# Optimization experiments

Measured on AMD Instinct MI355X. Metric: run time of the kernel, lower is better.

Reference implementation:

```python
import math
import jax, jax.numpy as jnp
import numpy as np

B, S, T = 16, 1024, 2048
C, Fdim = 128, 20          # C*Fdim = 2560 (q in_features)
PH_DIM = 512               # k/v in_features
OUT_DIM = 512              # out_dim
MEL_DIM = 20 * 64          # 1280


def setup_inputs() -> dict:
    key = jax.random.key(0)
    ks = jax.random.split(key, 12)
    ph = jax.random.normal(ks[0], (B, S, PH_DIM), dtype=jnp.float32)
    g = jax.random.normal(ks[1], (B, C, Fdim, T), dtype=jnp.float32)
    lengths = jax.random.randint(ks[2], (B,), 1, S + 1, dtype=jnp.int64)
    def lin(k, fan_in, fan_out):
        bound = 1.0 / math.sqrt(fan_in)
        kw, kb = jax.random.split(k)
        W = jax.random.uniform(kw, (fan_in, fan_out), jnp.float32, -bound, bound)
        b = jax.random.uniform(kb, (fan_out,), jnp.float32, -bound, bound)
        return W, b
    Wk, bk = lin(ks[3], PH_DIM, OUT_DIM)
    Wv, bv = lin(ks[4], PH_DIM, OUT_DIM)
    Wq, bq = lin(ks[5], C * Fdim, OUT_DIM)
    Wmel, bmel = lin(ks[6], OUT_DIM, MEL_DIM)
    return {"ph": ph, "g": g, "lengths": lengths,
            "Wk": Wk, "bk": bk, "Wv": Wv, "bv": bv,
            "Wq": Wq, "bq": bq, "Wmel": Wmel, "bmel": bmel}


def reference(ph, g, lengths, Wk, bk, Wv, bv, Wq, bq, Wmel, bmel):
    b, c, f, t = g.shape
    d = Wk.shape[1]
    k = ph @ Wk + bk                              # [B,S,D]
    q = g.reshape(b, c * f, t).transpose(0, 2, 1) @ Wq + bq  # [B,T,D]
    att = jnp.einsum('btd,bsd->bts', q, k) / math.sqrt(d)    # [B,T,S]
    valid = jnp.arange(k.shape[1])[None, None, :] < lengths[:, None, None]
    att = jnp.where(valid, att, -jnp.inf)
    att = jax.nn.softmax(att, axis=2)
    v = ph @ Wv + bv                              # [B,S,D]
    value = jnp.einsum('bts,bsd->btd', att, v)    # [B,T,D]
    out = value @ Wmel + bmel                     # [B,T,1280]
    out = out.reshape(b, t, f, -1).transpose(0, 3, 2, 1)  # [B,64,F,T]
    return out
```

## Files before the change

### kernel.cpp

```cpp
#include <hip/hip_runtime.h>
#include <stdint.h>


typedef __attribute__((ext_vector_type(4))) float f32x4;
typedef __attribute__((ext_vector_type(8))) short bf16x8;

#define AS1 __attribute__((address_space(1)))
#define AS3 __attribute__((address_space(3)))

__device__ __forceinline__ ushort f2b(float x) {
    union { float f; uint32_t u; } v; v.f = x;
    uint32_t r = (v.u + 0x7FFFu + ((v.u >> 16) & 1u)) >> 16;
    return (ushort)r;
}
__device__ __forceinline__ float b2f(ushort u) {
    union { uint32_t u; float f; } v; v.u = ((uint32_t)u) << 16;
    return v.f;
}

__device__ __forceinline__ void gload16(const void* g, void* l) {
    __builtin_amdgcn_global_load_lds((const AS1 uint32_t*)g,
                                     (AS3 uint32_t*)l, 16, 0, 0);
}

__global__ void sniff_dtype(const uint32_t* __restrict__ ph, int* __restrict__ flag)
{
    if (threadIdx.x == 0 && blockIdx.x == 0) {
        int cnt = 0;
        for (int i = 0; i < 64; ++i) {
            uint32_t e = (ph[i] >> 7) & 0xFFu;
            if (e >= 90u && e <= 140u) ++cnt;
        }
        *flag = (cnt >= 40) ? 1 : 0;
    }
}


__global__ __launch_bounds__(256)
void cvt_bias(const void* __restrict__ src, float* __restrict__ dst, int n,
              const int* __restrict__ flag)
{
    int i = blockIdx.x * 256 + threadIdx.x;
    if (i >= n) return;
    dst[i] = (*flag == 0) ? ((const float*)src)[i]
                          : b2f(((const ushort*)src)[i]);
}

__global__ __launch_bounds__(256)
void cvt_bf16(const void* __restrict__ src, ushort* __restrict__ dst, int n8,
              const int* __restrict__ flag)
{
    int i = blockIdx.x * 256 + threadIdx.x;
    if (i >= n8) return;
    if (*flag == 0) {
        const float4* s = (const float4*)src;
        float4 a = s[2 * i], b = s[2 * i + 1];
        uint4 o;
        o.x = (uint32_t)f2b(a.x) | ((uint32_t)f2b(a.y) << 16);
        o.y = (uint32_t)f2b(a.z) | ((uint32_t)f2b(a.w) << 16);
        o.z = (uint32_t)f2b(b.x) | ((uint32_t)f2b(b.y) << 16);
        o.w = (uint32_t)f2b(b.z) | ((uint32_t)f2b(b.w) << 16);
        ((uint4*)dst)[i] = o;
    } else {
        ((uint4*)dst)[i] = ((const uint4*)src)[i];
    }
}

__global__ __launch_bounds__(256)
void transpose_cvt(const void* __restrict__ src, ushort* __restrict__ dst,
                   int R, int Cc, long sbat, long dbat,
                   const int* __restrict__ flag)
{
    __shared__ ushort tile[32][33];
    const bool isf32 = (*flag == 0);
    const int r0 = blockIdx.y * 32, c0 = blockIdx.x * 32;
    const int tr = threadIdx.x >> 3;
    const int tc4 = (threadIdx.x & 7) * 4;

    const char* sb = (const char*)src + (size_t)blockIdx.z * sbat * (isf32 ? 4 : 2);
    if (isf32) {
        const float4* s = (const float4*)((const float*)sb + (size_t)(r0 + tr) * Cc + c0 + tc4);
        float4 v = *s;
        tile[tr][tc4 + 0] = f2b(v.x); tile[tr][tc4 + 1] = f2b(v.y);
        tile[tr][tc4 + 2] = f2b(v.z); tile[tr][tc4 + 3] = f2b(v.w);
    } else {
        const ushort4* s = (const ushort4*)((const ushort*)sb + (size_t)(r0 + tr) * Cc + c0 + tc4);
        ushort4 v = *s;
        tile[tr][tc4 + 0] = v.x; tile[tr][tc4 + 1] = v.y;
        tile[tr][tc4 + 2] = v.z; tile[tr][tc4 + 3] = v.w;
    }
    __syncthreads();
    ushort4 o;
    o.x = tile[tc4 + 0][tr]; o.y = tile[tc4 + 1][tr];
    o.z = tile[tc4 + 2][tr]; o.w = tile[tc4 + 3][tr];
    *(ushort4*)(dst + (size_t)blockIdx.z * dbat + (size_t)(c0 + tr) * R + r0 + tc4) = o;
}

template<int STORE>
__global__ __launch_bounds__(256)
void mfma_gemm(const ushort* __restrict__ A, const ushort* __restrict__ Bt,
               void* __restrict__ C, const float* __restrict__ bias,
               int M, int N, int K,
               long Abat, long Bbat, long Cbat, long ldc, float scale)
{
    __shared__ ushort As[128 * 32];
    __shared__ ushort Bs[128 * 32];

    const int tid = threadIdx.x;
    const int lane = tid & 63;
    const int wave = tid >> 6;
    const int wr = wave >> 1, wc = wave & 1;
    const int m0 = blockIdx.y * 128, n0 = blockIdx.x * 128;

    const ushort* Ab = A + (size_t)blockIdx.z * Abat;
    const ushort* Bb = Bt + (size_t)blockIdx.z * Bbat;

    const int srow = tid >> 2;
    const int scol = (tid & 3) * 8;
    const ushort* gA = Ab + (size_t)(m0 + srow) * K + scol;
    const ushort* gB = Bb + (size_t)(n0 + srow) * K + scol;
    const size_t rowskip = (size_t)64 * K;
    ushort* lA = As + tid * 8;
    ushort* lB = Bs + tid * 8;

    const int fr = lane & 15;
    const int fk = (lane >> 4) * 8;
    const ushort* pa = As + (size_t)(wr * 64 + fr) * 32 + fk;
    const ushort* pb = Bs + (size_t)(wc * 64 + fr) * 32 + fk;

    f32x4 acc[4][4] = {};

    for (int k0 = 0; k0 < K; k0 += 32) {
        gload16(gA, lA);
        gload16(gA + rowskip, lA + 2048);
        gload16(gB, lB);
        gload16(gB + rowskip, lB + 2048);
        gA += 32; gB += 32;
        __syncthreads();

        bf16x8 af[4], bf[4];
#pragma unroll
        for (int i = 0; i < 4; ++i) af[i] = *(const bf16x8*)(pa + (size_t)i * 16 * 32);
#pragma unroll
        for (int i = 0; i < 4; ++i) bf[i] = *(const bf16x8*)(pb + (size_t)i * 16 * 32);
#pragma unroll
        for (int mi = 0; mi < 4; ++mi)
#pragma unroll
            for (int ni = 0; ni < 4; ++ni)
                acc[mi][ni] = __builtin_amdgcn_mfma_f32_16x16x32_bf16(
                    af[mi], bf[ni], acc[mi][ni], 0, 0, 0);
        __syncthreads();
    }

    const int nb = n0 + wc * 64;
    const int mb = m0 + wr * 64 + (lane >> 4) * 4;
#pragma unroll
    for (int ni = 0; ni < 4; ++ni) {
        const int n = nb + ni * 16 + fr;
        const float bv = bias ? bias[n] : 0.f;
#pragma unroll
        for (int mi = 0; mi < 4; ++mi) {
            f32x4 v = acc[mi][ni];
            const int m = mb + mi * 16;
            if (STORE == 0) {
                ushort* Cc = (ushort*)C + (size_t)blockIdx.z * Cbat;
#pragma unroll
                for (int r = 0; r < 4; ++r)
                    Cc[(size_t)(m + r) * ldc + n] = f2b(v[r] * scale + bv);
            } else if (STORE == 1) {
                ushort* Cc = (ushort*)C + (size_t)blockIdx.z * Cbat;
                ushort4 o;
                o.x = f2b(v[0] * scale + bv); o.y = f2b(v[1] * scale + bv);
                o.z = f2b(v[2] * scale + bv); o.w = f2b(v[3] * scale + bv);
                *(ushort4*)(Cc + (size_t)n * ldc + m) = o;
            } else {
                float* Cf = (float*)C + (size_t)blockIdx.z * Cbat;
                float4 o = { v[0] * scale + bv, v[1] * scale + bv,
                             v[2] * scale + bv, v[3] * scale + bv };
                *(float4*)(Cf + (size_t)(n & 63) * (20 * 2048)
                              + (size_t)(n >> 6) * 2048 + m) = o;
            }
        }
    }
}

__global__ __launch_bounds__(256)
void softmax_mask(ushort* __restrict__ sc, const int* __restrict__ lengths)
{
    const int t = blockIdx.x, b = blockIdx.y, tid = threadIdx.x;
    const bool is64 = (lengths[1] == 0 && lengths[3] == 0 && lengths[5] == 0);
    const int len = is64 ? lengths[2 * b] : lengths[b];

    ushort* row = sc + ((size_t)b * 2048 + t) * 1024;
    const int s0 = tid * 4;
    uint2 pk = *(const uint2*)(row + s0);
    ushort u[4] = { (ushort)(pk.x & 0xffff), (ushort)(pk.x >> 16),
                    (ushort)(pk.y & 0xffff), (ushort)(pk.y >> 16) };
    float v[4];
    float mx = -INFINITY;
#pragma unroll
    for (int j = 0; j < 4; ++j) {
        v[j] = (s0 + j < len) ? b2f(u[j]) : -INFINITY;
        mx = fmaxf(mx, v[j]);
    }
    for (int off = 32; off > 0; off >>= 1) mx = fmaxf(mx, __shfl_xor(mx, off));
    __shared__ float redm[4], reds[4];
    const int w = tid >> 6;
    if ((tid & 63) == 0) redm[w] = mx;
    __syncthreads();
    mx = fmaxf(fmaxf(redm[0], redm[1]), fmaxf(redm[2], redm[3]));

    float e[4]; float sum = 0.f;
#pragma unroll
    for (int j = 0; j < 4; ++j) { e[j] = __expf(v[j] - mx); sum += e[j]; }
    for (int off = 32; off > 0; off >>= 1) sum += __shfl_xor(sum, off);
    if ((tid & 63) == 0) reds[w] = sum;
    __syncthreads();
    sum = reds[0] + reds[1] + reds[2] + reds[3];
    const float inv = 1.0f / sum;

    ushort o[4];
#pragma unroll
    for (int j = 0; j < 4; ++j) o[j] = f2b(e[j] * inv);
    uint2 opk;
    opk.x = (uint32_t)o[0] | ((uint32_t)o[1] << 16);
    opk.y = (uint32_t)o[2] | ((uint32_t)o[3] << 16);
    *(uint2*)(row + s0) = opk;
}

extern "C" void kernel_launch(void* const* d_in, const int* in_sizes, int n_in,
                              void* d_out, int out_size, void* d_ws, size_t ws_size,
                              hipStream_t stream)
{
    const void* ph   = d_in[0];
    const void* g    = d_in[1];
    const int*  len  = (const int*)d_in[2];
    const void* Wk   = d_in[3];
    const void* bk   = d_in[4];
    const void* Wv   = d_in[5];
    const void* bv   = d_in[6];
    const void* Wq   = d_in[7];
    const void* bq   = d_in[8];
    const void* Wmel = d_in[9];
    const void* bmel = d_in[10];
    void* out = d_out;

    char* ws = (char*)d_ws;
    size_t off = 0;
    auto alloc = [&](size_t bytes) -> char* {
        char* p = ws + off;
        off += (bytes + 255) & ~(size_t)255;
        return p;
    };
    int*    flag  = (int*)alloc(256);
    float*  bkf   = (float*)alloc(512 * 4);
    float*  bvf   = (float*)alloc(512 * 4);
    float*  bqf   = (float*)alloc(512 * 4);
    float*  bmelf = (float*)alloc(1280 * 4);
    ushort* WkT   = (ushort*)alloc((size_t)512 * 512 * 2);
    ushort* WvT   = (ushort*)alloc((size_t)512 * 512 * 2);
    ushort* WqT   = (ushort*)alloc((size_t)512 * 2560 * 2);
    ushort* WmelT = (ushort*)alloc((size_t)1280 * 512 * 2);
    ushort* qval  = (ushort*)alloc((size_t)16 * 2048 * 512 * 2);

    char* dob = (char*)d_out;
    ushort* gT  = (ushort*)dob;
    ushort* phb = (ushort*)dob;
    ushort* kbf = (ushort*)(dob + 16777216);
    ushort* vT  = (ushort*)(dob + 33554432);
    ushort* sc  = (ushort*)(dob + 50331648);

    sniff_dtype<<<1, 64, 0, stream>>>((const uint32_t*)ph, flag);

    transpose_cvt<<<dim3(64, 80, 16), 256, 0, stream>>>(
        g, gT, 2560, 2048, 2560L * 2048, 2560L * 2048, flag);
    transpose_cvt<<<dim3(16, 16, 1), 256, 0, stream>>>(Wk, WkT, 512, 512, 0, 0, flag);
    transpose_cvt<<<dim3(16, 16, 1), 256, 0, stream>>>(Wv, WvT, 512, 512, 0, 0, flag);
    transpose_cvt<<<dim3(16, 80, 1), 256, 0, stream>>>(Wq, WqT, 2560, 512, 0, 0, flag);
    transpose_cvt<<<dim3(40, 16, 1), 256, 0, stream>>>(Wmel, WmelT, 512, 1280, 0, 0, flag);
    cvt_bias<<<2, 256, 0, stream>>>(bk, bkf, 512, flag);
    cvt_bias<<<2, 256, 0, stream>>>(bv, bvf, 512, flag);
    cvt_bias<<<2, 256, 0, stream>>>(bq, bqf, 512, flag);
    cvt_bias<<<5, 256, 0, stream>>>(bmel, bmelf, 1280, flag);

    mfma_gemm<0><<<dim3(4, 16, 16), 256, 0, stream>>>(
        gT, WqT, qval, bqf, 2048, 512, 2560,
        2048L * 2560, 0, 2048L * 512, 512, 1.f);

    cvt_bf16<<<4096, 256, 0, stream>>>(ph, phb, 1048576, flag);

    mfma_gemm<0><<<dim3(4, 8, 16), 256, 0, stream>>>(
        phb, WkT, kbf, bkf, 1024, 512, 512,
        1024L * 512, 0, 1024L * 512, 512, 1.f);
    mfma_gemm<1><<<dim3(4, 8, 16), 256, 0, stream>>>(
        phb, WvT, vT, bvf, 1024, 512, 512,
        1024L * 512, 0, 512L * 1024, 1024, 1.f);

    mfma_gemm<0><<<dim3(8, 16, 16), 256, 0, stream>>>(
        qval, kbf, sc, nullptr, 2048, 1024, 512,
        2048L * 512, 1024L * 512, 2048L * 1024, 1024, 0.044194173824159216f);

    softmax_mask<<<dim3(2048, 16), 256, 0, stream>>>(sc, len);

    mfma_gemm<0><<<dim3(4, 16, 16), 256, 0, stream>>>(
        sc, vT, qval, nullptr, 2048, 512, 1024,
        2048L * 1024, 512L * 1024, 2048L * 512, 512, 1.f);

    mfma_gemm<2><<<dim3(10, 16, 16), 256, 0, stream>>>(
        qval, WmelT, out, bmelf, 2048, 1280, 512,
        2048L * 512, 0, 64L * 20 * 2048, 0, 1.f);
}
```

Baseline: 1.000 ms.

## Fuse g transpose and conversion into a dedicated Q-projection GEMM kernel

Removes the separate transpose_cvt pass over g (16x2560x2048) and the generic Q GEMM. A new 512-thread kernel reads g directly in its native [C*F, T] layout, converts it to bf16 in registers and feeds MFMA, with WqT double-buffered in LDS through global_load_lds. This avoids writing and re-reading a large intermediate. The cost is strided per-element global loads of g (16 lanes contiguous), high register pressure from 32 accumulators plus 32 raw values, and only 256 blocks in the grid.

```diff
diff --git a/kernel.cpp b/kernel.cpp
--- a/kernel.cpp
+++ b/kernel.cpp
@@ -94,6 +94,138 @@
     o.x = tile[tc4 + 0][tr]; o.y = tile[tc4 + 1][tr];
     o.z = tile[tc4 + 2][tr]; o.w = tile[tc4 + 3][tr];
     *(ushort4*)(dst + (size_t)blockIdx.z * dbat + (size_t)(c0 + tr) * R + r0 + tc4) = o;
+}
+
+__global__ __launch_bounds__(512, 2)
+void qproj_fused(const void* __restrict__ G, const ushort* __restrict__ WqT,
+                 ushort* __restrict__ Q, const float* __restrict__ bq,
+                 const int* __restrict__ flag)
+{
+    __shared__ ushort Bs[2][512 * 32];
+    const bool isf32 = (*flag == 0);
+    const int tid = threadIdx.x;
+    const int lane = tid & 63;
+    const int wave = tid >> 6;
+    const int wr = wave >> 2, wc = wave & 3;
+    const int fr = lane & 15, fkg = lane >> 4;
+    const int m0 = blockIdx.x * 128;
+    const int bz = blockIdx.y;
+
+    const float*  gzf = (const float*)G  + (size_t)bz * 2560 * 2048;
+    const ushort* gzh = (const ushort*)G + (size_t)bz * 2560 * 2048;
+    const int mcol = m0 + wr * 64 + fr;
+
+    uint32_t idx[8];
+#pragma unroll
+    for (int j = 0; j < 8; ++j)
+        idx[j] = (uint32_t)(fkg * 8 + j) * 2048u + (uint32_t)mcol;
+
+    const ushort* gB[4];
+#pragma unroll
+    for (int p = 0; p < 4; ++p)
+        gB[p] = WqT + (size_t)((tid >> 2) + p * 128) * 2560 + (tid & 3) * 8;
+
+    float  rawf[4][8];
+    ushort rawh[4][8];
+
+    if (isf32) {
+#pragma unroll
+        for (int j = 0; j < 8; ++j)
+#pragma unroll
+            for (int mi = 0; mi < 4; ++mi)
+                rawf[mi][j] = gzf[idx[j] + mi * 16];
+    } else {
+#pragma unroll
+        for (int j = 0; j < 8; ++j)
+#pragma unroll
+            for (int mi = 0; mi < 4; ++mi)
+                rawh[mi][j] = gzh[idx[j] + mi * 16];
+    }
+#pragma unroll
+    for (int j = 0; j < 8; ++j) idx[j] += 65536u;
+
+#pragma unroll
+    for (int p = 0; p < 4; ++p)
+        gload16(gB[p], &Bs[0][tid * 8 + p * 4096]);
+
+    f32x4 acc[4][8] = {};
+
+    for (int kt = 0; kt < 80; ++kt) {
+        __syncthreads();
+
+        bf16x8 af[4];
+        if (isf32) {
+#pragma unroll
+            for (int mi = 0; mi < 4; ++mi) {
+                union { bf16x8 v; uint32_t u[4]; } w;
+#pragma unroll
+                for (int p = 0; p < 4; ++p)
+                    w.u[p] = (uint32_t)f2b(rawf[mi][2 * p]) |
+                             ((uint32_t)f2b(rawf[mi][2 * p + 1]) << 16);
+                af[mi] = w.v;
+            }
+        } else {
+#pragma unroll
+            for (int mi = 0; mi < 4; ++mi) {
+                union { bf16x8 v; uint32_t u[4]; } w;
+#pragma unroll
+                for (int p = 0; p < 4; ++p)
+                    w.u[p] = (uint32_t)rawh[mi][2 * p] |
+                             ((uint32_t)rawh[mi][2 * p + 1] << 16);
+                af[mi] = w.v;
+            }
+        }
+
+        if (kt + 1 < 80) {
+            if (isf32) {
+#pragma unroll
+                for (int j = 0; j < 8; ++j)
+#pragma unroll
+                    for (int mi = 0; mi < 4; ++mi)
+                        rawf[mi][j] = gzf[idx[j] + mi * 16];
+            } else {
+#pragma unroll
+                for (int j = 0; j < 8; ++j)
+#pragma unroll
+                    for (int mi = 0; mi < 4; ++mi)
+                        rawh[mi][j] = gzh[idx[j] + mi * 16];
+            }
+#pragma unroll
+            for (int j = 0; j < 8; ++j) idx[j] += 65536u;
+#pragma unroll
+            for (int p = 0; p < 4; ++p)
+                gload16(gB[p] + (kt + 1) * 32,
+                        &Bs[(kt + 1) & 1][tid * 8 + p * 4096]);
+        }
+
+        const ushort* pbb = &Bs[kt & 1][(wc * 128 + fr) * 32 + fkg * 8];
+        bf16x8 bfr[8];
+#pragma unroll
+        for (int ni = 0; ni < 8; ++ni)
+            bfr[ni] = *(const bf16x8*)(pbb + (size_t)ni * 16 * 32);
+
+#pragma unroll
+        for (int mi = 0; mi < 4; ++mi)
+#pragma unroll
+            for (int ni = 0; ni < 8; ++ni)
+                acc[mi][ni] = __builtin_amdgcn_mfma_f32_16x16x32_bf16(
+                    af[mi], bfr[ni], acc[mi][ni], 0, 0, 0);
+    }
+
+    ushort* qp = Q + (size_t)bz * 2048 * 512;
+#pragma unroll
+    for (int ni = 0; ni < 8; ++ni) {
+        const int n = wc * 128 + ni * 16 + fr;
+        const float bv = bq[n];
+#pragma unroll
+        for (int mi = 0; mi < 4; ++mi) {
+            f32x4 v = acc[mi][ni];
+            const int m = m0 + wr * 64 + mi * 16 + fkg * 4;
+#pragma unroll
+            for (int r = 0; r < 4; ++r)
+                qp[(size_t)(m + r) * 512 + n] = f2b(v[r] + bv);
+        }
+    }
 }
 
 template<int STORE>
@@ -264,7 +396,6 @@
     ushort* qval  = (ushort*)alloc((size_t)16 * 2048 * 512 * 2);
 
     char* dob = (char*)d_out;
-    ushort* gT  = (ushort*)dob;
     ushort* phb = (ushort*)dob;
     ushort* kbf = (ushort*)(dob + 16777216);
     ushort* vT  = (ushort*)(dob + 33554432);
@@ -272,8 +403,6 @@
 
     sniff_dtype<<<1, 64, 0, stream>>>((const uint32_t*)ph, flag);
 
-    transpose_cvt<<<dim3(64, 80, 16), 256, 0, stream>>>(
-        g, gT, 2560, 2048, 2560L * 2048, 2560L * 2048, flag);
     transpose_cvt<<<dim3(16, 16, 1), 256, 0, stream>>>(Wk, WkT, 512, 512, 0, 0, flag);
     transpose_cvt<<<dim3(16, 16, 1), 256, 0, stream>>>(Wv, WvT, 512, 512, 0, 0, flag);
     transpose_cvt<<<dim3(16, 80, 1), 256, 0, stream>>>(Wq, WqT, 2560, 512, 0, 0, flag);
@@ -282,31 +411,28 @@
     cvt_bias<<<2, 256, 0, stream>>>(bv, bvf, 512, flag);
     cvt_bias<<<2, 256, 0, stream>>>(bq, bqf, 512, flag);
     cvt_bias<<<5, 256, 0, stream>>>(bmel, bmelf, 1280, flag);
-
-    mfma_gemm<0><<<dim3(4, 16, 16), 256, 0, stream>>>(
-        gT, WqT, qval, bqf, 2048, 512, 2560,
-        2048L * 2560, 0, 2048L * 512, 512, 1.f);
-
     cvt_bf16<<<4096, 256, 0, stream>>>(ph, phb, 1048576, flag);
 
-    mfma_gemm<0><<<dim3(4, 8, 16), 256, 0, stream>>>(
+    qproj_fused<<<dim3(16, 16), 512, 0, stream>>>(g, WqT, qval, bqf, flag);
+
+    mfma_gemm<0><<<dim3(4, 8, 16), dim3(256), 0, stream>>>(
         phb, WkT, kbf, bkf, 1024, 512, 512,
         1024L * 512, 0, 1024L * 512, 512, 1.f);
-    mfma_gemm<1><<<dim3(4, 8, 16), 256, 0, stream>>>(
+    mfma_gemm<1><<<dim3(4, 8, 16), dim3(256), 0, stream>>>(
         phb, WvT, vT, bvf, 1024, 512, 512,
         1024L * 512, 0, 512L * 1024, 1024, 1.f);
 
-    mfma_gemm<0><<<dim3(8, 16, 16), 256, 0, stream>>>(
+    mfma_gemm<0><<<dim3(8, 16, 16), dim3(256), 0, stream>>>(
         qval, kbf, sc, nullptr, 2048, 1024, 512,
         2048L * 512, 1024L * 512, 2048L * 1024, 1024, 0.044194173824159216f);
 
     softmax_mask<<<dim3(2048, 16), 256, 0, stream>>>(sc, len);
 
-    mfma_gemm<0><<<dim3(4, 16, 16), 256, 0, stream>>>(
+    mfma_gemm<0><<<dim3(4, 16, 16), dim3(256), 0, stream>>>(
         sc, vT, qval, nullptr, 2048, 512, 1024,
         2048L * 1024, 512L * 1024, 2048L * 512, 512, 1.f);
 
-    mfma_gemm<2><<<dim3(10, 16, 16), 256, 0, stream>>>(
+    mfma_gemm<2><<<dim3(10, 16, 16), dim3(256), 0, stream>>>(
         qval, WmelT, out, bmelf, 2048, 1280, 512,
         2048L * 512, 0, 64L * 20 * 2048, 0, 1.f);
 }
```

Result: slower. 1.370 ms (+37.0%).

## Fuse g transpose and bf16 conversion into a dedicated Q-projection GEMM

Applied to the files above, without the earlier changes.

Drops the separate transpose_cvt pass over g (16x2560x2048) and the generic Q GEMM. A new qproj_fused2 kernel reads g directly in its native [C*F, T] layout, converts to bf16 and writes a padded LDS tile, then runs MFMA with 128x256 tiles. This avoids writing and re-reading a large transposed intermediate, but the A loads are strided per element rather than vectorized, there is no global-to-LDS async load for A, and the 128-accumulator tile per wave raises register pressure.

```diff
diff --git a/kernel.cpp b/kernel.cpp
--- a/kernel.cpp
+++ b/kernel.cpp
@@ -96,6 +96,92 @@
     *(ushort4*)(dst + (size_t)blockIdx.z * dbat + (size_t)(c0 + tr) * R + r0 + tc4) = o;
 }
 
+__global__ __launch_bounds__(256)
+void qproj_fused2(const void* __restrict__ G, const ushort* __restrict__ WqT,
+                  ushort* __restrict__ Q, const float* __restrict__ bq,
+                  const int* __restrict__ flag)
+{
+    __shared__ __align__(16) ushort As[128 * 40];
+    __shared__ __align__(16) ushort Bs[256 * 32];
+
+    const bool isf32 = (*flag == 0);
+    const int tid = threadIdx.x;
+    const int lane = tid & 63;
+    const int wave = tid >> 6;
+    const int wr = wave >> 1, wc = wave & 1;
+    const int n0 = blockIdx.x * 256;
+    const int m0 = blockIdx.y * 128;
+    const int bz = blockIdx.z;
+
+    const float*  gzf = (const float*)G  + (size_t)bz * 2560 * 2048;
+    const ushort* gzh = (const ushort*)G + (size_t)bz * 2560 * 2048;
+
+    const ushort* gB = WqT + (size_t)(n0 + (tid >> 2)) * 2560 + (tid & 3) * 8;
+    ushort* lB = Bs + tid * 8;
+    const size_t brs = (size_t)64 * 2560;
+
+    const int fr = lane & 15, fkg = lane >> 4;
+    const ushort* pa = As + (size_t)(wr * 64 + fr) * 40 + fkg * 8;
+    const ushort* pb = Bs + (size_t)(wc * 128 + fr) * 32 + fkg * 8;
+
+    f32x4 acc[4][8] = {};
+
+    for (int kt = 0; kt < 80; ++kt) {
+        const int k0 = kt * 32;
+        gload16(gB,           lB);
+        gload16(gB + brs,     lB + 2048);
+        gload16(gB + 2 * brs, lB + 4096);
+        gload16(gB + 3 * brs, lB + 6144);
+        gB += 32;
+#pragma unroll
+        for (int r = 0; r < 4; ++r) {
+            const int m  = lane + 64 * (r & 1);
+            const int kb = (wave + 4 * (r >> 1)) * 4;
+            ushort4 o;
+            if (isf32) {
+                const float* p = gzf + (size_t)(k0 + kb) * 2048 + m0 + m;
+                o.x = f2b(p[0]);    o.y = f2b(p[2048]);
+                o.z = f2b(p[4096]); o.w = f2b(p[6144]);
+            } else {
+                const ushort* p = gzh + (size_t)(k0 + kb) * 2048 + m0 + m;
+                o.x = p[0];    o.y = p[2048];
+                o.z = p[4096]; o.w = p[6144];
+            }
+            *(ushort4*)(As + (size_t)m * 40 + kb) = o;
+        }
+        __syncthreads();
+
+        bf16x8 af[4], bf[8];
+#pragma unroll
+        for (int i = 0; i < 4; ++i) af[i] = *(const bf16x8*)(pa + (size_t)i * 16 * 40);
+#pragma unroll
+        for (int i = 0; i < 8; ++i) bf[i] = *(const bf16x8*)(pb + (size_t)i * 16 * 32);
+#pragma unroll
+        for (int mi = 0; mi < 4; ++mi)
+#pragma unroll
+            for (int ni = 0; ni < 8; ++ni)
+                acc[mi][ni] = __builtin_amdgcn_mfma_f32_16x16x32_bf16(
+                    af[mi], bf[ni], acc[mi][ni], 0, 0, 0);
+        __syncthreads();
+    }
+
+    ushort* qp = Q + (size_t)bz * 2048 * 512;
+    const int mb = m0 + wr * 64 + fkg * 4;
+#pragma unroll
+    for (int ni = 0; ni < 8; ++ni) {
+        const int n = n0 + wc * 128 + ni * 16 + fr;
+        const float bv = bq[n];
+#pragma unroll
+        for (int mi = 0; mi < 4; ++mi) {
+            f32x4 v = acc[mi][ni];
+            const int m = mb + mi * 16;
+#pragma unroll
+            for (int r = 0; r < 4; ++r)
+                qp[(size_t)(m + r) * 512 + n] = f2b(v[r] + bv);
+        }
+    }
+}
+
 template<int STORE>
 __global__ __launch_bounds__(256)
 void mfma_gemm(const ushort* __restrict__ A, const ushort* __restrict__ Bt,
@@ -103,8 +189,8 @@
                int M, int N, int K,
                long Abat, long Bbat, long Cbat, long ldc, float scale)
 {
-    __shared__ ushort As[128 * 32];
-    __shared__ ushort Bs[128 * 32];
+    __shared__ __align__(16) ushort As[128 * 32];
+    __shared__ __align__(16) ushort Bs[128 * 32];
 
     const int tid = threadIdx.x;
     const int lane = tid & 63;
@@ -264,7 +350,6 @@
     ushort* qval  = (ushort*)alloc((size_t)16 * 2048 * 512 * 2);
 
     char* dob = (char*)d_out;
-    ushort* gT  = (ushort*)dob;
     ushort* phb = (ushort*)dob;
     ushort* kbf = (ushort*)(dob + 16777216);
     ushort* vT  = (ushort*)(dob + 33554432);
@@ -272,8 +357,6 @@
 
     sniff_dtype<<<1, 64, 0, stream>>>((const uint32_t*)ph, flag);
 
-    transpose_cvt<<<dim3(64, 80, 16), 256, 0, stream>>>(
-        g, gT, 2560, 2048, 2560L * 2048, 2560L * 2048, flag);
     transpose_cvt<<<dim3(16, 16, 1), 256, 0, stream>>>(Wk, WkT, 512, 512, 0, 0, flag);
     transpose_cvt<<<dim3(16, 16, 1), 256, 0, stream>>>(Wv, WvT, 512, 512, 0, 0, flag);
     transpose_cvt<<<dim3(16, 80, 1), 256, 0, stream>>>(Wq, WqT, 2560, 512, 0, 0, flag);
@@ -282,31 +365,28 @@
     cvt_bias<<<2, 256, 0, stream>>>(bv, bvf, 512, flag);
     cvt_bias<<<2, 256, 0, stream>>>(bq, bqf, 512, flag);
     cvt_bias<<<5, 256, 0, stream>>>(bmel, bmelf, 1280, flag);
-
-    mfma_gemm<0><<<dim3(4, 16, 16), 256, 0, stream>>>(
-        gT, WqT, qval, bqf, 2048, 512, 2560,
-        2048L * 2560, 0, 2048L * 512, 512, 1.f);
-
     cvt_bf16<<<4096, 256, 0, stream>>>(ph, phb, 1048576, flag);
 
-    mfma_gemm<0><<<dim3(4, 8, 16), 256, 0, stream>>>(
+    qproj_fused2<<<dim3(2, 16, 16), 256, 0, stream>>>(g, WqT, qval, bqf, flag);
+
+    mfma_gemm<0><<<dim3(4, 8, 16), dim3(256), 0, stream>>>(
         phb, WkT, kbf, bkf, 1024, 512, 512,
         1024L * 512, 0, 1024L * 512, 512, 1.f);
-    mfma_gemm<1><<<dim3(4, 8, 16), 256, 0, stream>>>(
+    mfma_gemm<1><<<dim3(4, 8, 16), dim3(256), 0, stream>>>(
         phb, WvT, vT, bvf, 1024, 512, 512,
         1024L * 512, 0, 512L * 1024, 1024, 1.f);
 
-    mfma_gemm<0><<<dim3(8, 16, 16), 256, 0, stream>>>(
+    mfma_gemm<0><<<dim3(8, 16, 16), dim3(256), 0, stream>>>(
         qval, kbf, sc, nullptr, 2048, 1024, 512,
         2048L * 512, 1024L * 512, 2048L * 1024, 1024, 0.044194173824159216f);
 
     softmax_mask<<<dim3(2048, 16), 256, 0, stream>>>(sc, len);
 
-    mfma_gemm<0><<<dim3(4, 16, 16), 256, 0, stream>>>(
+    mfma_gemm<0><<<dim3(4, 16, 16), dim3(256), 0, stream>>>(
         sc, vT, qval, nullptr, 2048, 512, 1024,
         2048L * 1024, 512L * 1024, 2048L * 512, 512, 1.f);
 
-    mfma_gemm<2><<<dim3(10, 16, 16), 256, 0, stream>>>(
+    mfma_gemm<2><<<dim3(10, 16, 16), dim3(256), 0, stream>>>(
         qval, WmelT, out, bmelf, 2048, 1280, 512,
         2048L * 512, 0, 64L * 20 * 2048, 0, 1.f);
 }
```

Measured after the change: 1.343 ms. 34.3% more time.
